# Performance work log

Measured on AMD Instinct MI355X. Metric: run time of the kernel, lower is better.

## Reference

```python
import jax, jax.numpy as jnp
import numpy as np

N_NODES = 50000
N_EDGES = 1600000
D_IN = 192   # n_features + n_graphfea
D_HID = 128


def _gcn_conv(x, W, b, src, dst, dhis, n):
    """GCNConv returning two views.
    view1: symmetric-normalized propagation with self-loops (standard GCN).
    view2: raw neighbor sum of transformed features (to be scaled by D_inv outside).
    dhis: deg_hat^{-1/2} per node, deg_hat = in-degree + 1 (self loop).
    """
    h = x @ W + b                                      # [N, hid]
    w = dhis[src] * dhis[dst]                          # [E] edge norm
    view1 = jax.ops.segment_sum(h[src] * w[:, None], dst, num_segments=n)
    view1 = view1 + h * (dhis * dhis)[:, None]         # self-loop term
    view2 = jax.ops.segment_sum(h[src], dst, num_segments=n)
    return view1, view2


def setup_inputs() -> dict:
    key = jax.random.key(0)
    ks = jax.random.split(key, 12)
    x = jax.random.normal(ks[0], (N_NODES, D_IN), dtype=jnp.float32)
    view2 = jax.random.normal(ks[1], (N_NODES, D_IN), dtype=jnp.float32)
    edge_index = jax.random.randint(ks[2], (2, N_EDGES), 0, N_NODES, dtype=jnp.int64)
    D_inv = jax.random.uniform(ks[3], (N_NODES, 1), dtype=jnp.float32)
    def glorot(k, fan_in, fan_out):
        s = jnp.sqrt(jnp.float32(2.0 / (fan_in + fan_out)))
        return jax.random.normal(k, (fan_in, fan_out), dtype=jnp.float32) * s
    W1 = glorot(ks[4], D_IN, D_HID)
    W2 = glorot(ks[5], D_HID, D_HID)
    W3 = glorot(ks[6], D_HID, D_HID)
    W4 = glorot(ks[7], D_IN, D_HID)
    W5 = glorot(ks[8], D_HID, D_HID)
    W6 = glorot(ks[9], D_HID, D_HID)
    z = jnp.zeros((D_HID,), dtype=jnp.float32)
    return {"x": x, "view2": view2, "edge_index": edge_index, "D_inv": D_inv,
            "W1": W1, "b1": z, "W2": W2, "b2": z, "W3": W3, "b3": z,
            "W4": W4, "b4": z, "W5": W5, "b5": z, "W6": W6, "b6": z}


def reference(x, view2, edge_index, D_inv,
              W1, b1, W2, b2, W3, b3, W4, b4, W5, b5, W6, b6):
    n = x.shape[0]
    src, dst = edge_index[0], edge_index[1]
    deg = jax.ops.segment_sum(jnp.ones_like(dst, dtype=x.dtype), dst, num_segments=n)
    dhis = jax.lax.rsqrt(deg + 1.0)                    # deg_hat^{-1/2}
    relu = jax.nn.relu

    x1v1, x1v2 = _gcn_conv(x, W1, b1, src, dst, dhis, n)
    x2v1, x2v2 = _gcn_conv(view2, W4, b4, src, dst, dhis, n)
    x1 = relu(x1v1 + x2v2 * D_inv)
    x2 = relu(x2v1 + x1v2 * D_inv)

    z1v1, z1v2 = _gcn_conv(x1, W2, b2, src, dst, dhis, n)
    z2v1, z2v2 = _gcn_conv(x2, W5, b5, src, dst, dhis, n)
    z1 = relu(z1v1 + z2v2 * D_inv)
    z2 = relu(z2v1 + z1v2 * D_inv)

    v1v1, v1v2 = _gcn_conv(z1, W3, b3, src, dst, dhis, n)
    v2v1, v2v2 = _gcn_conv(z2, W6, b6, src, dst, dhis, n)
    v1 = relu(v1v1 + v2v2 * D_inv)
    v2 = relu(v2v1 + v1v2 * D_inv)

    q = jnp.concatenate([x1, z1, v1], axis=1)          # [N, 3*hid]
    p = jnp.concatenate([x2, z2, v2], axis=1)
    return q, p
```

## Files before the change

kernel.cpp:

```cpp
#include <hip/hip_runtime.h>

#define N_NODES 50000
#define N_EDGES 1600000
#define D_IN 192
#define D_HID 128

#define NSLICE 8
#define SLICE_SZ ((N_NODES + NSLICE - 1) / NSLICE)

#define NW_TOTAL 114688
#define SCAN_BLOCKS ((N_NODES + 255) / 256)

typedef __bf16 bf16x8 __attribute__((ext_vector_type(8)));
typedef float f32x4 __attribute__((ext_vector_type(4)));
typedef float f32x2 __attribute__((ext_vector_type(2)));
typedef unsigned short u16x8 __attribute__((ext_vector_type(8)));

__device__ __forceinline__ unsigned short f2b(float x) {
    unsigned u = __builtin_bit_cast(unsigned, x);
    u += 0x7FFFu + ((u >> 16) & 1u);
    return (unsigned short)(u >> 16);
}
__device__ __forceinline__ float blo(unsigned u) {
    return __builtin_bit_cast(float, u << 16);
}
__device__ __forceinline__ float bhi(unsigned u) {
    return __builtin_bit_cast(float, u & 0xFFFF0000u);
}
__device__ __forceinline__ bf16x8 pack8(float4 a, float4 b) {
    u16x8 t;
    t[0] = f2b(a.x); t[1] = f2b(a.y); t[2] = f2b(a.z); t[3] = f2b(a.w);
    t[4] = f2b(b.x); t[5] = f2b(b.y); t[6] = f2b(b.z); t[7] = f2b(b.w);
    return __builtin_bit_cast(bf16x8, t);
}


__global__ __launch_bounds__(256) void prep_zero(
        const float* __restrict__ W1, const float* __restrict__ W4,
        const float* __restrict__ W2, const float* __restrict__ W3,
        const float* __restrict__ W5, const float* __restrict__ W6,
        unsigned short* __restrict__ Wt,
        int* __restrict__ cnt, unsigned long long* __restrict__ part) {
    int idx = blockIdx.x * 256 + threadIdx.x;
    if (idx < N_NODES) cnt[idx] = 0;
    if (idx < 256) part[idx] = 0ULL;
    if (idx < NW_TOTAL) {
        const float* W; int K, base;
        if      (idx <  24576) { W = W1; K = 192; base = 0; }
        else if (idx <  49152) { W = W4; K = 192; base = 24576; }
        else if (idx <  65536) { W = W2; K = 128; base = 49152; }
        else if (idx <  81920) { W = W3; K = 128; base = 65536; }
        else if (idx <  98304) { W = W5; K = 128; base = 81920; }
        else                   { W = W6; K = 128; base = 98304; }
        int r = idx - base;
        int j = r / K, k = r - j * K;
        Wt[idx] = f2b(W[(size_t)k * 128 + j]);
    }
}


__global__ void hist_kernel(const int* __restrict__ dst, int E,
                            int* __restrict__ cnt, int* __restrict__ rank) {
    int e = blockIdx.x * blockDim.x + threadIdx.x;
    if (e < E) rank[e] = atomicAdd(&cnt[dst[e]], 1);
}


#define AGG_FLAG (1ULL << 62)
#define INCL_FLAG (2ULL << 62)
#define VAL_MASK 0xFFFFFFFFULL

__global__ __launch_bounds__(256) void scan_lb(
        const int* __restrict__ cnt,
        unsigned long long* __restrict__ part,
        int* __restrict__ row_ptr, float* __restrict__ dhis) {
    __shared__ int ls[256];
    __shared__ int bofs;
    int tid = threadIdx.x, bid = blockIdx.x;
    int i = bid * 256 + tid;
    int c = (i < N_NODES) ? cnt[i] : 0;
    ls[tid] = c;
    __syncthreads();
    for (int off = 1; off < 256; off <<= 1) {
        int add = (tid >= off) ? ls[tid - off] : 0;
        __syncthreads();
        ls[tid] += add;
        __syncthreads();
    }
    int T = ls[255];

    if (tid == 0) {
        if (bid == 0) {
            atomicExch(part + 0, (unsigned long long)T | INCL_FLAG);
            bofs = 0;
        } else {
            atomicExch(part + bid, (unsigned long long)T | AGG_FLAG);
        }
    }

    if (bid > 0 && tid < 64) {
        int lane = tid;
        int running = 0;
        int w = bid;
        while (true) {
            int j = w - 64 + lane;
            unsigned long long v = 0;
            bool active = (j >= 0);
            if (active) {
                do { v = atomicAdd(part + j, 0ULL); } while ((v >> 62) == 0);
            }
            unsigned long long ball = __ballot(active && ((v >> 62) == 2));
            int contrib;
            bool done;
            if (ball) {
                int hi = 63 - __clzll(ball);
                contrib = (lane >= hi && active) ? (int)(v & VAL_MASK) : 0;
                done = true;
            } else {
                contrib = active ? (int)(v & VAL_MASK) : 0;
                done = false;
            }
#pragma unroll
            for (int o = 32; o > 0; o >>= 1) contrib += __shfl_down(contrib, o);
            running += __shfl(contrib, 0);
            if (done) break;
            w -= 64;
        }
        if (lane == 0) {
            atomicExch(part + bid, (unsigned long long)(running + T) | INCL_FLAG);
            bofs = running;
        }
    }
    __syncthreads();
    int run = (bid == 0) ? 0 : bofs;
    if (i < N_NODES) {
        row_ptr[i] = run + ls[tid] - c;
        dhis[i] = rsqrtf((float)c + 1.0f);
        if (i == N_NODES - 1) row_ptr[N_NODES] = run + ls[tid];
    }
}


__global__ __launch_bounds__(256) void fill_sliced(
        const int* __restrict__ src, const int* __restrict__ dst,
        const int* __restrict__ rank, const int* __restrict__ row_ptr,
        int* __restrict__ esrc, int E, int nchunks) {
    int slice = blockIdx.x & (NSLICE - 1);
    int chunk = blockIdx.x >> 3;
    int lo = slice * SLICE_SZ;
    int hi = lo + SLICE_SZ;
    int per = (E + nchunks - 1) / nchunks;
    int e0 = chunk * per;
    int e1 = min(e0 + per, E);
    for (int e = e0 + threadIdx.x; e < e1; e += 256) {
        int d = dst[e];
        if (d >= lo && d < hi) {
            esrc[row_ptr[d] + rank[e]] = src[e];
        }
    }
}


__global__ __launch_bounds__(256) void gemm_dual(
        const float* __restrict__ A0, const float* __restrict__ A1, int lda,
        int K, int ns,
        const unsigned short* __restrict__ Wt0, const unsigned short* __restrict__ Wt1,
        const float* __restrict__ bias0, const float* __restrict__ bias1,
        unsigned short* __restrict__ out, int M) {
    __shared__ __align__(16) unsigned short Wlds[192 * 128];

    int view = blockIdx.y;
    const float* A = view ? A1 : A0;
    const unsigned short* Wt = view ? Wt1 : Wt0;
    const float* bias = view ? bias1 : bias0;

    int tid = threadIdx.x;

    int nfrag = ns * 512;
    for (int f = tid; f < nfrag; f += 256) {
        int lane = f & 63;
        int gk = f >> 6;
        int g = gk / ns, ks = gk - g * ns;
        int col = g * 16 + (lane & 15);
        int kpos = ks * 32 + (lane >> 4) * 8;
        *(bf16x8*)(Wlds + (size_t)f * 8) =
            *(const bf16x8*)(Wt + (size_t)col * K + kpos);
    }
    __syncthreads();

    int wave = tid >> 6, lane = tid & 63;
    int m = lane & 15, quad = lane >> 4;
    int row0 = blockIdx.x * 128;

    int rA0 = row0 + wave * 32 + m;
    int rA1 = rA0 + 16;
    int cA0 = rA0 < M ? rA0 : M - 1;
    int cA1 = rA1 < M ? rA1 : M - 1;
    const float* a0 = A + (size_t)cA0 * lda + quad * 8;
    const float* a1 = A + (size_t)cA1 * lda + quad * 8;

    f32x4 acc[2][8];
#pragma unroll
    for (int h = 0; h < 2; ++h)
#pragma unroll
        for (int g = 0; g < 8; ++g) acc[h][g] = (f32x4){0.f, 0.f, 0.f, 0.f};

    const bf16x8* wl = (const bf16x8*)Wlds;
    for (int ks = 0; ks < ns; ++ks) {
        float4 va = *(const float4*)(a0 + ks * 32);
        float4 vb = *(const float4*)(a0 + ks * 32 + 4);
        float4 vc = *(const float4*)(a1 + ks * 32);
        float4 vd = *(const float4*)(a1 + ks * 32 + 4);
        bf16x8 af0 = pack8(va, vb);
        bf16x8 af1 = pack8(vc, vd);
#pragma unroll
        for (int g = 0; g < 8; ++g) {
            bf16x8 bfr = wl[(g * ns + ks) * 64 + lane];
            acc[0][g] = __builtin_amdgcn_mfma_f32_16x16x32_bf16(af0, bfr, acc[0][g], 0, 0, 0);
            acc[1][g] = __builtin_amdgcn_mfma_f32_16x16x32_bf16(af1, bfr, acc[1][g], 0, 0, 0);
        }
    }

#pragma unroll
    for (int h = 0; h < 2; ++h) {
#pragma unroll
        for (int g = 0; g < 8; ++g) {
            int col = g * 16 + m;
            float bv = bias[col];
            int ci = ((col >> 1) << 2) + (view << 1) + (col & 1);
#pragma unroll
            for (int r = 0; r < 4; ++r) {
                int grow = row0 + wave * 32 + h * 16 + quad * 4 + r;
                if (grow < M) out[(size_t)grow * 256 + ci] = f2b(acc[h][g][r] + bv);
            }
        }
    }
}


__global__ __launch_bounds__(256) void agg_kernel(
        const unsigned* __restrict__ hcomb,
        const int* __restrict__ row_ptr, const int* __restrict__ esrc,
        const float* __restrict__ dhis, const float* __restrict__ D_inv,
        float* __restrict__ out_q, float* __restrict__ out_p, int n) {
    int wave = threadIdx.x >> 6, lane = threadIdx.x & 63;
    int d = blockIdx.x * 4 + wave;
    if (d >= n) return;

    const uint2* hc2 = (const uint2*)hcomb;

    int e0 = row_ptr[d], e1 = row_ptr[d + 1];
    f32x2 a1 = {0.f, 0.f}, g1 = {0.f, 0.f};
    f32x2 a2 = {0.f, 0.f}, g2 = {0.f, 0.f};

#define EDGE_BODY(u, w) {                                         \
        f32x2 v1 = {blo((u).x), bhi((u).x)};                      \
        f32x2 v2 = {blo((u).y), bhi((u).y)};                      \
        f32x2 wv = {(w), (w)};                                    \
        a1 += v1; g1 = __builtin_elementwise_fma(v1, wv, g1);     \
        a2 += v2; g2 = __builtin_elementwise_fma(v2, wv, g2); }

    int e = e0;
    for (; e + 8 <= e1; e += 8) {
        int4 sa = *(const int4*)(esrc + e);
        int4 sb = *(const int4*)(esrc + e + 4);
        uint2 u0 = hc2[((size_t)sa.x << 6) + lane];
        uint2 u1 = hc2[((size_t)sa.y << 6) + lane];
        uint2 u2 = hc2[((size_t)sa.z << 6) + lane];
        uint2 u3 = hc2[((size_t)sa.w << 6) + lane];
        uint2 u4 = hc2[((size_t)sb.x << 6) + lane];
        uint2 u5 = hc2[((size_t)sb.y << 6) + lane];
        uint2 u6 = hc2[((size_t)sb.z << 6) + lane];
        uint2 u7 = hc2[((size_t)sb.w << 6) + lane];
        float w0 = dhis[sa.x], w1 = dhis[sa.y], w2 = dhis[sa.z], w3 = dhis[sa.w];
        float w4 = dhis[sb.x], w5 = dhis[sb.y], w6 = dhis[sb.z], w7 = dhis[sb.w];
        EDGE_BODY(u0, w0); EDGE_BODY(u1, w1);
        EDGE_BODY(u2, w2); EDGE_BODY(u3, w3);
        EDGE_BODY(u4, w4); EDGE_BODY(u5, w5);
        EDGE_BODY(u6, w6); EDGE_BODY(u7, w7);
    }
    for (; e + 4 <= e1; e += 4) {
        int4 sa = *(const int4*)(esrc + e);
        uint2 u0 = hc2[((size_t)sa.x << 6) + lane];
        uint2 u1 = hc2[((size_t)sa.y << 6) + lane];
        uint2 u2 = hc2[((size_t)sa.z << 6) + lane];
        uint2 u3 = hc2[((size_t)sa.w << 6) + lane];
        float w0 = dhis[sa.x], w1 = dhis[sa.y], w2 = dhis[sa.z], w3 = dhis[sa.w];
        EDGE_BODY(u0, w0); EDGE_BODY(u1, w1);
        EDGE_BODY(u2, w2); EDGE_BODY(u3, w3);
    }
    for (; e < e1; ++e) {
        int s = esrc[e];
        uint2 u = hc2[((size_t)s << 6) + lane];
        EDGE_BODY(u, dhis[s]);
    }
#undef EDGE_BODY

    float dh = dhis[d];
    float di = D_inv[d];
    float dh2 = dh * dh;
    f32x2 dhv = {dh, dh}, dh2v = {dh2, dh2}, div = {di, di};

    uint2 us = hc2[((size_t)d << 6) + lane];
    f32x2 s1 = {blo(us.x), bhi(us.x)};
    f32x2 s2 = {blo(us.y), bhi(us.y)};

    f32x2 o1 = __builtin_elementwise_fma(g1, dhv,
               __builtin_elementwise_fma(s1, dh2v, a2 * div));
    f32x2 o2 = __builtin_elementwise_fma(g2, dhv,
               __builtin_elementwise_fma(s2, dh2v, a1 * div));

    f32x2 zero = {0.f, 0.f};
    o1 = __builtin_elementwise_max(o1, zero);
    o2 = __builtin_elementwise_max(o2, zero);
    *(f32x2*)(out_q + (size_t)d * 384 + lane * 2) = o1;
    *(f32x2*)(out_p + (size_t)d * 384 + lane * 2) = o2;
}


extern "C" void kernel_launch(void* const* d_in, const int* in_sizes, int n_in,
                              void* d_out, int out_size, void* d_ws, size_t ws_size,
                              hipStream_t stream) {
    const float* x     = (const float*)d_in[0];
    const float* view2 = (const float*)d_in[1];
    const int*   eidx  = (const int*)d_in[2];
    const float* D_inv = (const float*)d_in[3];
    const float* W1 = (const float*)d_in[4];  const float* b1 = (const float*)d_in[5];
    const float* W2 = (const float*)d_in[6];  const float* b2 = (const float*)d_in[7];
    const float* W3 = (const float*)d_in[8];  const float* b3 = (const float*)d_in[9];
    const float* W4 = (const float*)d_in[10]; const float* b4 = (const float*)d_in[11];
    const float* W5 = (const float*)d_in[12]; const float* b5 = (const float*)d_in[13];
    const float* W6 = (const float*)d_in[14]; const float* b6 = (const float*)d_in[15];

    const int n = N_NODES;
    const int E = N_EDGES;
    const int* src  = eidx;
    const int* dstv = eidx + E;

    char* ws = (char*)d_ws;
    size_t off = 0;
    auto alloc = [&](size_t bytes) -> void* {
        void* p = ws + off;
        off += (bytes + 255) & ~(size_t)255;
        return p;
    };
    int*   cnt     = (int*)alloc((size_t)n * 4);
    int*   row_ptr = (int*)alloc((size_t)(n + 1) * 4);
    float* dhis    = (float*)alloc((size_t)n * 4);
    int*   rank    = (int*)alloc((size_t)E * 4);
    int*   esrc    = (int*)alloc((size_t)E * 4);
    unsigned long long* part = (unsigned long long*)alloc((size_t)256 * 8);
    unsigned short* hcomb = (unsigned short*)alloc((size_t)n * 256 * 2);
    unsigned short* Wta   = (unsigned short*)alloc((size_t)NW_TOTAL * 2);

    unsigned short* Wt1 = Wta + 0;
    unsigned short* Wt4 = Wta + 24576;
    unsigned short* Wt2 = Wta + 49152;
    unsigned short* Wt3 = Wta + 65536;
    unsigned short* Wt5 = Wta + 81920;
    unsigned short* Wt6 = Wta + 98304;

    float* qb = (float*)d_out;
    float* pb = qb + (size_t)n * 384;

    int eblocks = (E + 255) / 256;
    prep_zero<<<(NW_TOTAL + 255) / 256, 256, 0, stream>>>(W1, W4, W2, W3, W5, W6,
                                                          Wta, cnt, part);
    hist_kernel<<<eblocks, 256, 0, stream>>>(dstv, E, cnt, rank);
    scan_lb<<<SCAN_BLOCKS, 256, 0, stream>>>(cnt, part, row_ptr, dhis);
    int nchunks = 1024;
    fill_sliced<<<nchunks * NSLICE, 256, 0, stream>>>(src, dstv, rank, row_ptr,
                                                      esrc, E, nchunks);

    dim3 ggrid((n + 127) / 128, 2);
    int ablocks = (n + 3) / 4;
    const unsigned* hc = (const unsigned*)hcomb;

    gemm_dual<<<ggrid, 256, 0, stream>>>(x, view2, D_IN, 192, 6, Wt1, Wt4, b1, b4, hcomb, n);
    agg_kernel<<<ablocks, 256, 0, stream>>>(hc, row_ptr, esrc, dhis, D_inv, qb + 0, pb + 0, n);

    gemm_dual<<<ggrid, 256, 0, stream>>>(qb, pb, 384, 128, 4, Wt2, Wt5, b2, b5, hcomb, n);
    agg_kernel<<<ablocks, 256, 0, stream>>>(hc, row_ptr, esrc, dhis, D_inv, qb + 128, pb + 128, n);

    gemm_dual<<<ggrid, 256, 0, stream>>>(qb + 128, pb + 128, 384, 128, 4, Wt3, Wt6, b3, b6, hcomb, n);
    agg_kernel<<<ablocks, 256, 0, stream>>>(hc, row_ptr, esrc, dhis, D_inv, qb + 256, pb + 256, n);
}
```

Baseline: 777.9 us.

## Fuse weight prep with histogram and fill CSR via atomic cursors

Merges the weight transpose/convert kernel and the degree histogram into one launch, with the count array zeroed by a memset. The per-edge rank array is dropped: the CSR fill now reserves slots with atomicAdd on a per-node cursor initialised by the scan, which removes a 6.4 MB write and read. Slice count drops from 8 to 4 and chunk count doubles. The trade-off is extra atomics during the fill and a nondeterministic edge order within each row.

```diff
diff --git a/kernel.cpp b/kernel.cpp
--- a/kernel.cpp
+++ b/kernel.cpp
@@ -5,11 +5,13 @@
 #define D_IN 192
 #define D_HID 128
 
-#define NSLICE 8
+#define NSLICE 4
 #define SLICE_SZ ((N_NODES + NSLICE - 1) / NSLICE)
 
 #define NW_TOTAL 114688
 #define SCAN_BLOCKS ((N_NODES + 255) / 256)
+#define PREP_BLOCKS (NW_TOTAL / 256)
+#define HIST_BLOCKS ((N_EDGES + 255) / 256)
 
 typedef __bf16 bf16x8 __attribute__((ext_vector_type(8)));
 typedef float f32x4 __attribute__((ext_vector_type(4)));
@@ -35,34 +37,33 @@
 }
 
 
-__global__ __launch_bounds__(256) void prep_zero(
+__global__ __launch_bounds__(256) void prep_hist(
         const float* __restrict__ W1, const float* __restrict__ W4,
         const float* __restrict__ W2, const float* __restrict__ W3,
         const float* __restrict__ W5, const float* __restrict__ W6,
         unsigned short* __restrict__ Wt,
-        int* __restrict__ cnt, unsigned long long* __restrict__ part) {
-    int idx = blockIdx.x * 256 + threadIdx.x;
-    if (idx < N_NODES) cnt[idx] = 0;
-    if (idx < 256) part[idx] = 0ULL;
-    if (idx < NW_TOTAL) {
-        const float* W; int K, base;
-        if      (idx <  24576) { W = W1; K = 192; base = 0; }
-        else if (idx <  49152) { W = W4; K = 192; base = 24576; }
-        else if (idx <  65536) { W = W2; K = 128; base = 49152; }
-        else if (idx <  81920) { W = W3; K = 128; base = 65536; }
-        else if (idx <  98304) { W = W5; K = 128; base = 81920; }
-        else                   { W = W6; K = 128; base = 98304; }
-        int r = idx - base;
-        int j = r / K, k = r - j * K;
-        Wt[idx] = f2b(W[(size_t)k * 128 + j]);
-    }
-}
-
-
-__global__ void hist_kernel(const int* __restrict__ dst, int E,
-                            int* __restrict__ cnt, int* __restrict__ rank) {
-    int e = blockIdx.x * blockDim.x + threadIdx.x;
-    if (e < E) rank[e] = atomicAdd(&cnt[dst[e]], 1);
+        const int* __restrict__ dst, int* __restrict__ cnt,
+        unsigned long long* __restrict__ part) {
+    int bid = blockIdx.x;
+    if (bid < PREP_BLOCKS) {
+        int idx = bid * 256 + threadIdx.x;
+        if (idx < 2048) part[idx] = 0ULL;
+        if (idx < NW_TOTAL) {
+            const float* W; int K, base;
+            if      (idx <  24576) { W = W1; K = 192; base = 0; }
+            else if (idx <  49152) { W = W4; K = 192; base = 24576; }
+            else if (idx <  65536) { W = W2; K = 128; base = 49152; }
+            else if (idx <  81920) { W = W3; K = 128; base = 65536; }
+            else if (idx <  98304) { W = W5; K = 128; base = 81920; }
+            else                   { W = W6; K = 128; base = 98304; }
+            int r = idx - base;
+            int j = r / K, k = r - j * K;
+            Wt[idx] = f2b(W[(size_t)k * 128 + j]);
+        }
+    } else {
+        int e = (bid - PREP_BLOCKS) * 256 + threadIdx.x;
+        if (e < N_EDGES) atomicAdd(&cnt[dst[e]], 1);
+    }
 }
 
 
@@ -73,7 +74,8 @@
 __global__ __launch_bounds__(256) void scan_lb(
         const int* __restrict__ cnt,
         unsigned long long* __restrict__ part,
-        int* __restrict__ row_ptr, float* __restrict__ dhis) {
+        int* __restrict__ row_ptr, int* __restrict__ fillcur,
+        float* __restrict__ dhis) {
     __shared__ int ls[256];
     __shared__ int bofs;
     int tid = threadIdx.x, bid = blockIdx.x;
@@ -134,19 +136,20 @@
     __syncthreads();
     int run = (bid == 0) ? 0 : bofs;
     if (i < N_NODES) {
-        row_ptr[i] = run + ls[tid] - c;
+        int pre = run + ls[tid] - c;
+        row_ptr[i] = pre;
+        fillcur[i] = pre;
         dhis[i] = rsqrtf((float)c + 1.0f);
         if (i == N_NODES - 1) row_ptr[N_NODES] = run + ls[tid];
     }
 }
 
 
-__global__ __launch_bounds__(256) void fill_sliced(
+__global__ __launch_bounds__(256) void fill_atomic(
         const int* __restrict__ src, const int* __restrict__ dst,
-        const int* __restrict__ rank, const int* __restrict__ row_ptr,
-        int* __restrict__ esrc, int E, int nchunks) {
+        int* __restrict__ fillcur, int* __restrict__ esrc, int E, int nchunks) {
     int slice = blockIdx.x & (NSLICE - 1);
-    int chunk = blockIdx.x >> 3;
+    int chunk = blockIdx.x >> 2;
     int lo = slice * SLICE_SZ;
     int hi = lo + SLICE_SZ;
     int per = (E + nchunks - 1) / nchunks;
@@ -155,7 +158,8 @@
     for (int e = e0 + threadIdx.x; e < e1; e += 256) {
         int d = dst[e];
         if (d >= lo && d < hi) {
-            esrc[row_ptr[d] + rank[e]] = src[e];
+            int slot = atomicAdd(&fillcur[d], 1);
+            esrc[slot] = src[e];
         }
     }
 }
@@ -346,10 +350,10 @@
     };
     int*   cnt     = (int*)alloc((size_t)n * 4);
     int*   row_ptr = (int*)alloc((size_t)(n + 1) * 4);
+    int*   fillcur = (int*)alloc((size_t)n * 4);
     float* dhis    = (float*)alloc((size_t)n * 4);
-    int*   rank    = (int*)alloc((size_t)E * 4);
     int*   esrc    = (int*)alloc((size_t)E * 4);
-    unsigned long long* part = (unsigned long long*)alloc((size_t)256 * 8);
+    unsigned long long* part = (unsigned long long*)alloc((size_t)2048 * 8);
     unsigned short* hcomb = (unsigned short*)alloc((size_t)n * 256 * 2);
     unsigned short* Wta   = (unsigned short*)alloc((size_t)NW_TOTAL * 2);
 
@@ -363,14 +367,13 @@
     float* qb = (float*)d_out;
     float* pb = qb + (size_t)n * 384;
 
-    int eblocks = (E + 255) / 256;
-    prep_zero<<<(NW_TOTAL + 255) / 256, 256, 0, stream>>>(W1, W4, W2, W3, W5, W6,
-                                                          Wta, cnt, part);
-    hist_kernel<<<eblocks, 256, 0, stream>>>(dstv, E, cnt, rank);
-    scan_lb<<<SCAN_BLOCKS, 256, 0, stream>>>(cnt, part, row_ptr, dhis);
-    int nchunks = 1024;
-    fill_sliced<<<nchunks * NSLICE, 256, 0, stream>>>(src, dstv, rank, row_ptr,
-                                                      esrc, E, nchunks);
+    hipMemsetAsync(cnt, 0, (size_t)n * 4, stream);
+    prep_hist<<<PREP_BLOCKS + HIST_BLOCKS, 256, 0, stream>>>(
+        W1, W4, W2, W3, W5, W6, Wta, dstv, cnt, part);
+    scan_lb<<<SCAN_BLOCKS, 256, 0, stream>>>(cnt, part, row_ptr, fillcur, dhis);
+    int nchunks = 2048;
+    fill_atomic<<<nchunks * NSLICE, 256, 0, stream>>>(src, dstv, fillcur, esrc,
+                                                      E, nchunks);
 
     dim3 ggrid((n + 127) / 128, 2);
     int ablocks = (n + 3) / 4;
```

Measured after the change: 813.5 us. 1.05x slower.

## Bucket CSR edges by source range within each destination for gather locality

Applied to the files above, without the earlier changes.

Builds the CSR with 8 source-range sub-buckets per destination node, so each row's edge list is partially sorted by source index. The aim is better L2/cache locality when the aggregation kernel gathers neighbor feature rows. In exchange the histogram, scan and fill operate on an array 8x larger than before (400k counters), which adds preprocessing cost and more scan blocks.

```diff
diff --git a/kernel.cpp b/kernel.cpp
--- a/kernel.cpp
+++ b/kernel.cpp
@@ -7,9 +7,13 @@
 
 #define NSLICE 8
 #define SLICE_SZ ((N_NODES + NSLICE - 1) / NSLICE)
+#define NSRC 8
+#define SRC_SL 6250
 
 #define NW_TOTAL 114688
-#define SCAN_BLOCKS ((N_NODES + 255) / 256)
+#define NB_TOT (N_NODES * NSRC)
+#define SCAN_BLOCKS ((NB_TOT + 255) / 256)
+#define PREP_BLOCKS 1563
 
 typedef __bf16 bf16x8 __attribute__((ext_vector_type(8)));
 typedef float f32x4 __attribute__((ext_vector_type(4)));
@@ -40,10 +44,10 @@
         const float* __restrict__ W2, const float* __restrict__ W3,
         const float* __restrict__ W5, const float* __restrict__ W6,
         unsigned short* __restrict__ Wt,
-        int* __restrict__ cnt, unsigned long long* __restrict__ part) {
+        int* __restrict__ cnt2, unsigned long long* __restrict__ part) {
     int idx = blockIdx.x * 256 + threadIdx.x;
-    if (idx < N_NODES) cnt[idx] = 0;
-    if (idx < 256) part[idx] = 0ULL;
+    if (idx < NB_TOT) cnt2[idx] = 0;
+    if (idx < SCAN_BLOCKS) part[idx] = 0ULL;
     if (idx < NW_TOTAL) {
         const float* W; int K, base;
         if      (idx <  24576) { W = W1; K = 192; base = 0; }
@@ -59,10 +63,13 @@
 }
 
 
-__global__ void hist_kernel(const int* __restrict__ dst, int E,
-                            int* __restrict__ cnt, int* __restrict__ rank) {
+__global__ void hist_kernel(const int* __restrict__ src, const int* __restrict__ dst,
+                            int E, int* __restrict__ cnt2, int* __restrict__ rank) {
     int e = blockIdx.x * blockDim.x + threadIdx.x;
-    if (e < E) rank[e] = atomicAdd(&cnt[dst[e]], 1);
+    if (e < E) {
+        int b = dst[e] * NSRC + src[e] / SRC_SL;
+        rank[e] = atomicAdd(&cnt2[b], 1);
+    }
 }
 
 
@@ -71,14 +78,14 @@
 #define VAL_MASK 0xFFFFFFFFULL
 
 __global__ __launch_bounds__(256) void scan_lb(
-        const int* __restrict__ cnt,
+        const int* __restrict__ cnt2,
         unsigned long long* __restrict__ part,
-        int* __restrict__ row_ptr, float* __restrict__ dhis) {
+        int* __restrict__ rp2, float* __restrict__ dhis) {
     __shared__ int ls[256];
     __shared__ int bofs;
     int tid = threadIdx.x, bid = blockIdx.x;
     int i = bid * 256 + tid;
-    int c = (i < N_NODES) ? cnt[i] : 0;
+    int c = (i < NB_TOT) ? cnt2[i] : 0;
     ls[tid] = c;
     __syncthreads();
     for (int off = 1; off < 256; off <<= 1) {
@@ -133,17 +140,20 @@
     }
     __syncthreads();
     int run = (bid == 0) ? 0 : bofs;
-    if (i < N_NODES) {
-        row_ptr[i] = run + ls[tid] - c;
-        dhis[i] = rsqrtf((float)c + 1.0f);
-        if (i == N_NODES - 1) row_ptr[N_NODES] = run + ls[tid];
+    if (i < NB_TOT) {
+        rp2[i] = run + ls[tid] - c;
+        if (i == NB_TOT - 1) rp2[NB_TOT] = run + ls[tid];
+        if ((tid & 7) == 7) {
+            int deg = ls[tid] - ((tid >= 8) ? ls[tid - 8] : 0);
+            dhis[i >> 3] = rsqrtf((float)deg + 1.0f);
+        }
     }
 }
 
 
 __global__ __launch_bounds__(256) void fill_sliced(
         const int* __restrict__ src, const int* __restrict__ dst,
-        const int* __restrict__ rank, const int* __restrict__ row_ptr,
+        const int* __restrict__ rank, const int* __restrict__ rp2,
         int* __restrict__ esrc, int E, int nchunks) {
     int slice = blockIdx.x & (NSLICE - 1);
     int chunk = blockIdx.x >> 3;
@@ -155,7 +165,8 @@
     for (int e = e0 + threadIdx.x; e < e1; e += 256) {
         int d = dst[e];
         if (d >= lo && d < hi) {
-            esrc[row_ptr[d] + rank[e]] = src[e];
+            int s = src[e];
+            esrc[rp2[d * NSRC + s / SRC_SL] + rank[e]] = s;
         }
     }
 }
@@ -240,7 +251,7 @@
 
 __global__ __launch_bounds__(256) void agg_kernel(
         const unsigned* __restrict__ hcomb,
-        const int* __restrict__ row_ptr, const int* __restrict__ esrc,
+        const int* __restrict__ rp2, const int* __restrict__ esrc,
         const float* __restrict__ dhis, const float* __restrict__ D_inv,
         float* __restrict__ out_q, float* __restrict__ out_p, int n) {
     int wave = threadIdx.x >> 6, lane = threadIdx.x & 63;
@@ -249,7 +260,7 @@
 
     const uint2* hc2 = (const uint2*)hcomb;
 
-    int e0 = row_ptr[d], e1 = row_ptr[d + 1];
+    int e0 = rp2[d * NSRC], e1 = rp2[d * NSRC + NSRC];
     f32x2 a1 = {0.f, 0.f}, g1 = {0.f, 0.f};
     f32x2 a2 = {0.f, 0.f}, g2 = {0.f, 0.f};
 
@@ -344,12 +355,12 @@
         off += (bytes + 255) & ~(size_t)255;
         return p;
     };
-    int*   cnt     = (int*)alloc((size_t)n * 4);
-    int*   row_ptr = (int*)alloc((size_t)(n + 1) * 4);
+    int*   cnt2    = (int*)alloc((size_t)NB_TOT * 4);
+    int*   rp2     = (int*)alloc((size_t)(NB_TOT + 1) * 4);
     float* dhis    = (float*)alloc((size_t)n * 4);
     int*   rank    = (int*)alloc((size_t)E * 4);
     int*   esrc    = (int*)alloc((size_t)E * 4);
-    unsigned long long* part = (unsigned long long*)alloc((size_t)256 * 8);
+    unsigned long long* part = (unsigned long long*)alloc((size_t)SCAN_BLOCKS * 8);
     unsigned short* hcomb = (unsigned short*)alloc((size_t)n * 256 * 2);
     unsigned short* Wta   = (unsigned short*)alloc((size_t)NW_TOTAL * 2);
 
@@ -364,12 +375,12 @@
     float* pb = qb + (size_t)n * 384;
 
     int eblocks = (E + 255) / 256;
-    prep_zero<<<(NW_TOTAL + 255) / 256, 256, 0, stream>>>(W1, W4, W2, W3, W5, W6,
-                                                          Wta, cnt, part);
-    hist_kernel<<<eblocks, 256, 0, stream>>>(dstv, E, cnt, rank);
-    scan_lb<<<SCAN_BLOCKS, 256, 0, stream>>>(cnt, part, row_ptr, dhis);
+    prep_zero<<<PREP_BLOCKS, 256, 0, stream>>>(W1, W4, W2, W3, W5, W6,
+                                               Wta, cnt2, part);
+    hist_kernel<<<eblocks, 256, 0, stream>>>(src, dstv, E, cnt2, rank);
+    scan_lb<<<SCAN_BLOCKS, 256, 0, stream>>>(cnt2, part, rp2, dhis);
     int nchunks = 1024;
-    fill_sliced<<<nchunks * NSLICE, 256, 0, stream>>>(src, dstv, rank, row_ptr,
+    fill_sliced<<<nchunks * NSLICE, 256, 0, stream>>>(src, dstv, rank, rp2,
                                                       esrc, E, nchunks);
 
     dim3 ggrid((n + 127) / 128, 2);
@@ -377,11 +388,11 @@
     const unsigned* hc = (const unsigned*)hcomb;
 
     gemm_dual<<<ggrid, 256, 0, stream>>>(x, view2, D_IN, 192, 6, Wt1, Wt4, b1, b4, hcomb, n);
-    agg_kernel<<<ablocks, 256, 0, stream>>>(hc, row_ptr, esrc, dhis, D_inv, qb + 0, pb + 0, n);
+    agg_kernel<<<ablocks, 256, 0, stream>>>(hc, rp2, esrc, dhis, D_inv, qb + 0, pb + 0, n);
 
     gemm_dual<<<ggrid, 256, 0, stream>>>(qb, pb, 384, 128, 4, Wt2, Wt5, b2, b5, hcomb, n);
-    agg_kernel<<<ablocks, 256, 0, stream>>>(hc, row_ptr, esrc, dhis, D_inv, qb + 128, pb + 128, n);
+    agg_kernel<<<ablocks, 256, 0, stream>>>(hc, rp2, esrc, dhis, D_inv, qb + 128, pb + 128, n);
 
     gemm_dual<<<ggrid, 256, 0, stream>>>(qb + 128, pb + 128, 384, 128, 4, Wt3, Wt6, b3, b6, hcomb, n);
-    agg_kernel<<<ablocks, 256, 0, stream>>>(hc, row_ptr, esrc, dhis, D_inv, qb + 256, pb + 256, n);
-}
+    agg_kernel<<<ablocks, 256, 0, stream>>>(hc, rp2, esrc, dhis, D_inv, qb + 256, pb + 256, n);
+}
```

Result: no change. 772.4 us (-0.7%).
